# Kernel tuning notes

Hardware: AMD Instinct MI355X
Metric: run time of the kernel (lower is better)

The kernel has to match this reference:

```python
import jax, jax.numpy as jnp
import numpy as np

IN_PLANES = 768
RATIO = 16


def setup_inputs() -> dict:
    key = jax.random.key(0)
    k1, k2, k3 = jax.random.split(key, 3)
    x = jax.random.normal(k1, (32, IN_PLANES, 56, 56), dtype=jnp.float32)
    hidden = IN_PLANES // RATIO
    # Conv2d(C, C//r, 1, bias=False) weight -> [C//r, C]; Conv2d(C//r, C, 1) -> [C, C//r]
    w1 = jax.random.normal(k2, (hidden, IN_PLANES), dtype=jnp.float32) * (1.0 / np.sqrt(IN_PLANES))
    w2 = jax.random.normal(k3, (IN_PLANES, hidden), dtype=jnp.float32) * (1.0 / np.sqrt(hidden))
    return {"x": x, "w1": w1, "w2": w2}


def _mlp(v, w1, w2):
    # v: [B, C]; shared 1x1-conv MLP with exact GELU (torch default)
    h = jax.nn.gelu(jnp.einsum("bc,hc->bh", v, w1), approximate=False)
    return jnp.einsum("bh,ch->bc", h, w2)


def reference(x, w1, w2):
    # x: [B, C, H, W]
    avg = jnp.mean(x, axis=(2, 3))  # [B, C]
    mx = jnp.max(x, axis=(2, 3))    # [B, C]
    gate = jax.nn.sigmoid(_mlp(avg, w1, w2) + _mlp(mx, w1, w2))  # [B, C]
    return x * gate[:, :, None, None]
```

## Files before the change

### kernel.cpp

```cpp
#include <hip/hip_runtime.h>
#include <math.h>

#define BATCH 32
#define CH 768
#define HW 3136
#define HW4 (HW/4)
#define HID 48
#define PLANES (BATCH*CH)

__global__ __launch_bounds__(256) void cbam_pool(const float* __restrict__ x,
                                                 float* __restrict__ avg,
                                                 float* __restrict__ mx) {
    const int plane = blockIdx.x;
    const float4* xp = reinterpret_cast<const float4*>(x + (size_t)plane * HW);

    float s = 0.0f;
    float m = -INFINITY;
    for (int i = threadIdx.x; i < HW4; i += 256) {
        float4 v = xp[i];
        s += v.x + v.y + v.z + v.w;
        m = fmaxf(m, fmaxf(fmaxf(v.x, v.y), fmaxf(v.z, v.w)));
    }
    for (int off = 32; off > 0; off >>= 1) {
        s += __shfl_down(s, off, 64);
        m = fmaxf(m, __shfl_down(m, off, 64));
    }
    __shared__ float ss[4];
    __shared__ float sm[4];
    const int wave = threadIdx.x >> 6;
    if ((threadIdx.x & 63) == 0) { ss[wave] = s; sm[wave] = m; }
    __syncthreads();
    if (threadIdx.x == 0) {
        float fs = ss[0] + ss[1] + ss[2] + ss[3];
        float fm = fmaxf(fmaxf(sm[0], sm[1]), fmaxf(sm[2], sm[3]));
        avg[plane] = fs * (1.0f / (float)HW);
        mx[plane]  = fm;
    }
}

__global__ __launch_bounds__(256) void cbam_mlp(const float* __restrict__ avg,
                                                const float* __restrict__ mx,
                                                const float* __restrict__ w1,
                                                const float* __restrict__ w2,
                                                float* __restrict__ gate) {
    const int b = blockIdx.x;
    __shared__ float sa[CH];
    __shared__ float sv[CH];
    __shared__ float ha[HID];
    __shared__ float hm[HID];
    __shared__ float hsum[HID];

    for (int i = threadIdx.x; i < CH; i += 256) {
        sa[i] = avg[b * CH + i];
        sv[i] = mx[b * CH + i];
    }
    __syncthreads();

    if (threadIdx.x < 2 * HID) {
        const bool is_avg = threadIdx.x < HID;
        const int h = is_avg ? threadIdx.x : threadIdx.x - HID;
        const float* in = is_avg ? sa : sv;
        const float* wr = w1 + (size_t)h * CH;
        float acc = 0.0f;
        #pragma unroll 8
        for (int k = 0; k < CH; ++k) acc += in[k] * wr[k];
        float g = 0.5f * acc * (1.0f + erff(acc * 0.70710678118654752f));
        if (is_avg) ha[h] = g; else hm[h] = g;
    }
    __syncthreads();
    if (threadIdx.x < HID) hsum[threadIdx.x] = ha[threadIdx.x] + hm[threadIdx.x];
    __syncthreads();

    for (int c = threadIdx.x; c < CH; c += 256) {
        const float* wr = w2 + (size_t)c * HID;
        float acc = 0.0f;
        #pragma unroll
        for (int h = 0; h < HID; ++h) acc += hsum[h] * wr[h];
        gate[b * CH + c] = 1.0f / (1.0f + expf(-acc));
    }
}

__global__ __launch_bounds__(256) void cbam_scale(const float* __restrict__ x,
                                                  const float* __restrict__ gate,
                                                  float* __restrict__ out) {
    const int plane = blockIdx.x;
    const float g = gate[plane];
    const float4* xp = reinterpret_cast<const float4*>(x + (size_t)plane * HW);
    float4* op = reinterpret_cast<float4*>(out + (size_t)plane * HW);
    for (int i = threadIdx.x; i < HW4; i += 256) {
        float4 v = xp[i];
        v.x *= g; v.y *= g; v.z *= g; v.w *= g;
        op[i] = v;
    }
}

extern "C" void kernel_launch(void* const* d_in, const int* in_sizes, int n_in,
                              void* d_out, int out_size, void* d_ws, size_t ws_size,
                              hipStream_t stream) {
    const float* x  = (const float*)d_in[0];
    const float* w1 = (const float*)d_in[1];
    const float* w2 = (const float*)d_in[2];
    float* out = (float*)d_out;

    float* avg  = (float*)d_ws;
    float* mx   = avg + PLANES;
    float* gate = mx + PLANES;

    cbam_pool<<<PLANES, 256, 0, stream>>>(x, avg, mx);
    cbam_mlp<<<BATCH, 256, 0, stream>>>(avg, mx, w1, w2, gate);
    cbam_scale<<<PLANES, 256, 0, stream>>>(x, gate, out);
}
```

Before: 208.1 us.

## Use one wave per plane, reverse scale order, nontemporal stores, vectorize MLP

```diff
diff --git a/kernel.cpp b/kernel.cpp
--- a/kernel.cpp
+++ b/kernel.cpp
@@ -7,34 +7,32 @@
 #define HW4 (HW/4)
 #define HID 48
 #define PLANES (BATCH*CH)
+#define WPB 4
+
+typedef float nfloat4 __attribute__((ext_vector_type(4)));
 
 __global__ __launch_bounds__(256) void cbam_pool(const float* __restrict__ x,
                                                  float* __restrict__ avg,
                                                  float* __restrict__ mx) {
-    const int plane = blockIdx.x;
-    const float4* xp = reinterpret_cast<const float4*>(x + (size_t)plane * HW);
+    const int wave = threadIdx.x >> 6;
+    const int lane = threadIdx.x & 63;
+    const int plane = blockIdx.x * WPB + wave;
+    const nfloat4* xp = reinterpret_cast<const nfloat4*>(x + (size_t)plane * HW);
 
     float s = 0.0f;
     float m = -INFINITY;
-    for (int i = threadIdx.x; i < HW4; i += 256) {
-        float4 v = xp[i];
-        s += v.x + v.y + v.z + v.w;
+    for (int i = lane; i < HW4; i += 64) {
+        nfloat4 v = xp[i];
+        s += (v.x + v.y) + (v.z + v.w);
         m = fmaxf(m, fmaxf(fmaxf(v.x, v.y), fmaxf(v.z, v.w)));
     }
     for (int off = 32; off > 0; off >>= 1) {
         s += __shfl_down(s, off, 64);
         m = fmaxf(m, __shfl_down(m, off, 64));
     }
-    __shared__ float ss[4];
-    __shared__ float sm[4];
-    const int wave = threadIdx.x >> 6;
-    if ((threadIdx.x & 63) == 0) { ss[wave] = s; sm[wave] = m; }
-    __syncthreads();
-    if (threadIdx.x == 0) {
-        float fs = ss[0] + ss[1] + ss[2] + ss[3];
-        float fm = fmaxf(fmaxf(sm[0], sm[1]), fmaxf(sm[2], sm[3]));
-        avg[plane] = fs * (1.0f / (float)HW);
-        mx[plane]  = fm;
+    if (lane == 0) {
+        avg[plane] = s * (1.0f / (float)HW);
+        mx[plane]  = m;
     }
 }
 
@@ -59,11 +57,15 @@
     if (threadIdx.x < 2 * HID) {
         const bool is_avg = threadIdx.x < HID;
         const int h = is_avg ? threadIdx.x : threadIdx.x - HID;
-        const float* in = is_avg ? sa : sv;
-        const float* wr = w1 + (size_t)h * CH;
+        const float4* in4 = reinterpret_cast<const float4*>(is_avg ? sa : sv);
+        const float4* wr4 = reinterpret_cast<const float4*>(w1 + (size_t)h * CH);
         float acc = 0.0f;
         #pragma unroll 8
-        for (int k = 0; k < CH; ++k) acc += in[k] * wr[k];
+        for (int k = 0; k < CH / 4; ++k) {
+            float4 a = in4[k];
+            float4 w = wr4[k];
+            acc += a.x * w.x + a.y * w.y + a.z * w.z + a.w * w.w;
+        }
         float g = 0.5f * acc * (1.0f + erff(acc * 0.70710678118654752f));
         if (is_avg) ha[h] = g; else hm[h] = g;
     }
@@ -72,10 +74,15 @@
     __syncthreads();
 
     for (int c = threadIdx.x; c < CH; c += 256) {
-        const float* wr = w2 + (size_t)c * HID;
+        const float4* wr4 = reinterpret_cast<const float4*>(w2 + (size_t)c * HID);
+        const float4* hs4 = reinterpret_cast<const float4*>(hsum);
         float acc = 0.0f;
         #pragma unroll
-        for (int h = 0; h < HID; ++h) acc += hsum[h] * wr[h];
+        for (int h = 0; h < HID / 4; ++h) {
+            float4 a = hs4[h];
+            float4 w = wr4[h];
+            acc += a.x * w.x + a.y * w.y + a.z * w.z + a.w * w.w;
+        }
         gate[b * CH + c] = 1.0f / (1.0f + expf(-acc));
     }
 }
@@ -83,14 +90,16 @@
 __global__ __launch_bounds__(256) void cbam_scale(const float* __restrict__ x,
                                                   const float* __restrict__ gate,
                                                   float* __restrict__ out) {
-    const int plane = blockIdx.x;
+    const int wave = threadIdx.x >> 6;
+    const int lane = threadIdx.x & 63;
+    const int plane = (PLANES - 1) - (blockIdx.x * WPB + wave);
     const float g = gate[plane];
-    const float4* xp = reinterpret_cast<const float4*>(x + (size_t)plane * HW);
-    float4* op = reinterpret_cast<float4*>(out + (size_t)plane * HW);
-    for (int i = threadIdx.x; i < HW4; i += 256) {
-        float4 v = xp[i];
+    const nfloat4* xp = reinterpret_cast<const nfloat4*>(x + (size_t)plane * HW);
+    nfloat4* op = reinterpret_cast<nfloat4*>(out + (size_t)plane * HW);
+    for (int i = lane; i < HW4; i += 64) {
+        nfloat4 v = xp[i];
         v.x *= g; v.y *= g; v.z *= g; v.w *= g;
-        op[i] = v;
+        __builtin_nontemporal_store(v, &op[i]);
     }
 }
 
@@ -106,7 +115,7 @@
     float* mx   = avg + PLANES;
     float* gate = mx + PLANES;
 
-    cbam_pool<<<PLANES, 256, 0, stream>>>(x, avg, mx);
+    cbam_pool<<<PLANES / WPB, 256, 0, stream>>>(x, avg, mx);
     cbam_mlp<<<BATCH, 256, 0, stream>>>(avg, mx, w1, w2, gate);
-    cbam_scale<<<PLANES, 256, 0, stream>>>(x, gate, out);
+    cbam_scale<<<PLANES / WPB, 256, 0, stream>>>(x, gate, out);
 }
```

New measurement: 175.7 us. 1.18x faster.
